# Optimization experiments

Measured on AMD Instinct MI355X. Metric: run time of the kernel, lower is better.

The kernel has to match this reference:

```python
import jax, jax.numpy as jnp
import numpy as np

B, L, A = 16, 32, 2046
M = A + 2  # user col + attributors + item col = 2048 nodes


def _xavier_uniform(key, shape, gain):
    fan_out, fan_in = shape  # torch 2D param: fan_in = shape[1], fan_out = shape[0]
    bound = gain * np.sqrt(6.0 / (fan_in + fan_out))
    return jax.random.uniform(key, shape, jnp.float32, -bound, bound)


def setup_inputs() -> dict:
    key = jax.random.key(0)
    k = jax.random.split(key, 7)
    user = jax.random.normal(k[0], (B, 6 * L, 1), jnp.float32)
    item = jax.random.normal(k[1], (B, 6 * L, 1), jnp.float32)
    attributor = jax.random.normal(k[2], (B, 6 * L, A), jnp.float32)
    adj = (jax.random.uniform(k[3], (M, M)) < 0.5).astype(jnp.float32)
    initial_weight = jax.random.normal(k[4], (M, M), jnp.float32)
    W_1 = _xavier_uniform(k[5], (6 * L, A), gain=np.sqrt(2.0))  # relu gain
    W_2 = _xavier_uniform(k[6], (6 * L, L), gain=1.44)
    return {"user": user, "item": item, "attributor": attributor,
            "adj": adj, "initial_weight": initial_weight,
            "W_1": W_1, "W_2": W_2}


def reference(user, item, attributor, adj, initial_weight, W_1, W_2):
    N = W_2.shape[1]  # = length L
    a = attributor * W_1                                   # (B, 6L, A)
    raw = jnp.concatenate([user, a, item], axis=2)         # (B, 6L, M)
    Q, K, V = jnp.split(raw, 3, axis=1)                    # each (B, 2L, M)
    r = jax.nn.relu
    # (relu(X).T @ W).T  ==  einsum over the 2L dim -> (B, L, M)
    Query = jnp.einsum('bnm,nl->blm', r(Q), W_2[:2 * N])
    Key = jnp.einsum('bnm,nl->blm', r(K), W_2[2 * N:4 * N])
    Value = jnp.einsum('bnm,nl->blm', r(V), W_2[4 * N:])
    # h = Query.mT @ Key * adj * initial_weight  -> (B, M, M)
    h = jnp.einsum('blm,bln->bmn', Query, Key) * adj * initial_weight
    d = h - jnp.swapaxes(h, -1, -2)
    exp_h = jnp.exp(jnp.where(d > 0, 0.0, d))              # exp(min(d, 0))
    causal = exp_h / (exp_h + jnp.swapaxes(exp_h, -1, -2)) * adj  # (B, M, M)
    Ans = Value @ causal                                    # (B, L, M)
    idx = jnp.array([0, Ans.shape[2] - 1])
    return Ans[:, :, idx]                                   # (B, L, 2)
```

## Files before the change

kernel.cpp:

```cpp
#include <hip/hip_runtime.h>
#include <math.h>

#define BB 16
#define LL 32
#define AA 2046
#define MM 2048
#define NROWS 192


__device__ __forceinline__ size_t Pidx(int rc, int j, int b, int n) {
  return ((size_t)(rc * 2 + j) * BB + b) * MM + n;
}

__global__ __launch_bounds__(256) void prep_kernel(
    const float* __restrict__ user, const float* __restrict__ item,
    const float* __restrict__ W2, float* __restrict__ uv,
    float* __restrict__ part) {
  const int b = blockIdx.x, t = threadIdx.x;
  __shared__ float KQ[4][LL];
  __shared__ float uvs[4][64];
  if (t < 128) {
    const int q = t >> 5, l = t & 31;
    const float* __restrict__ src = (q == 0 || q == 2) ? user : item;
    const int rbase = (q < 2) ? 64 : 0;
    float acc = 0.f;
#pragma unroll
    for (int r = 0; r < 64; ++r)
      acc += fmaxf(src[b * NROWS + rbase + r], 0.f) * W2[(rbase + r) * LL + l];
    KQ[q][l] = acc;
  }
  __syncthreads();
  {
    const int which = t >> 6, r = t & 63;
    const int wrow = (which < 2) ? r : 64 + r;
    float acc = 0.f;
#pragma unroll
    for (int l = 0; l < LL; ++l) acc += W2[wrow * LL + l] * KQ[which][l];
    uvs[which][r] = acc;
    uv[which * (BB * 64) + b * 64 + r] = acc;
  }
  __syncthreads();
  if (t < 8) {
    const int nsel = t & 1, j = (t >> 1) & 1, z = t >> 2;
    const float* __restrict__ src = nsel ? item : user;
    float acc = 0.f;
#pragma unroll
    for (int i = 0; i < 64; ++i)
      acc += fmaxf(src[b * NROWS + z * 64 + i], 0.f) * uvs[2 * z + j][i];
    const int n = nsel ? (MM - 1) : 0;
    part[Pidx(2 * z, j, b, n)] = acc;
    part[Pidx(2 * z + 1, j, b, n)] = 0.f;
  }
}

__global__ __launch_bounds__(256) void st_kernel(
    const float* __restrict__ att, const float* __restrict__ W1,
    const float* __restrict__ uv, float* __restrict__ part) {
  const int col = blockIdx.x * 256 + threadIdx.x;
  const int b = blockIdx.y, rc = blockIdx.z;
  if (col >= AA) return;
  const int z = rc >> 1;
  const float* __restrict__ w0 = uv + (2 * z) * (BB * 64) + b * 64;
  const float* __restrict__ w1 = uv + (2 * z + 1) * (BB * 64) + b * 64;
  const int r0 = rc * 32;
  float a0 = 0.f, a1 = 0.f;
#pragma unroll
  for (int i = 0; i < 32; ++i) {
    const int r = r0 + i;
    const float v =
        fmaxf(att[(size_t)(b * NROWS + r) * AA + col] * W1[(size_t)r * AA + col],
              0.f);
    const int wi = r - z * 64;
    a0 += v * w0[wi];
    a1 += v * w1[wi];
  }
  const int n = col + 1;
  part[Pidx(rc, 0, b, n)] = a0;
  part[Pidx(rc, 1, b, n)] = a1;
}

__global__ __launch_bounds__(256) void cweight_kernel(
    const float* __restrict__ adj, const float* __restrict__ iw,
    const float* __restrict__ part, float* __restrict__ c) {
  const int idx = blockIdx.x * 256 + threadIdx.x;
  const int b = idx >> 11, n = idx & (MM - 1);
  const float s0 = part[Pidx(0, 0, b, n)] + part[Pidx(1, 0, b, n)];
  const float s1 = part[Pidx(0, 1, b, n)] + part[Pidx(1, 1, b, n)];
  const float t0 = part[Pidx(2, 0, b, n)] + part[Pidx(3, 0, b, n)];
  const float t1 = part[Pidx(2, 1, b, n)] + part[Pidx(3, 1, b, n)];
  const float an0 = adj[(size_t)n * MM];
  const float an1 = adj[(size_t)n * MM + (MM - 1)];
  const float wn0 = an0 * iw[(size_t)n * MM];
  const float wn1 = an1 * iw[(size_t)n * MM + (MM - 1)];
  const float w0n = adj[n] * iw[n];
  const float w1n =
      adj[(size_t)(MM - 1) * MM + n] * iw[(size_t)(MM - 1) * MM + n];
  const float d0 = s0 * wn0 - t0 * w0n;
  const float d1 = s1 * wn1 - t1 * w1n;
  const float e0 = expf(-fabsf(d0));
  const float e1 = expf(-fabsf(d1));
  const float sig0 = (d0 > 0.f) ? 1.f / (1.f + e0) : e0 / (1.f + e0);
  const float sig1 = (d1 > 0.f) ? 1.f / (1.f + e1) : e1 / (1.f + e1);
  c[b * MM + n] = sig0 * an0;
  c[BB * MM + b * MM + n] = sig1 * an1;
}

__global__ __launch_bounds__(256) void gather_kernel(
    const float* __restrict__ user, const float* __restrict__ item,
    const float* __restrict__ att, const float* __restrict__ W1,
    const float* __restrict__ c, const float* __restrict__ W2,
    float* __restrict__ out) {
  const int rv = blockIdx.x, b = blockIdx.y, tid = threadIdx.x;
  const int r = 128 + rv;
  const int gr = b * NROWS + r;
  const float* __restrict__ c0 = c + b * MM;
  const float* __restrict__ c1 = c + BB * MM + b * MM;
  float g0 = 0.f, g1 = 0.f;
#pragma unroll
  for (int i = 0; i < 8; ++i) {
    const int col = i * 256 + tid;
    if (col < AA) {
      const float v = fmaxf(
          att[(size_t)gr * AA + col] * W1[(size_t)r * AA + col], 0.f);
      g0 += v * c0[col + 1];
      g1 += v * c1[col + 1];
    }
  }
  if (tid == 0) {
    const float uval = fmaxf(user[gr], 0.f);
    const float ival = fmaxf(item[gr], 0.f);
    g0 += uval * c0[0] + ival * c0[MM - 1];
    g1 += uval * c1[0] + ival * c1[MM - 1];
  }
  __shared__ float r0[256], r1[256];
  r0[tid] = g0;
  r1[tid] = g1;
  __syncthreads();
  for (int s = 128; s > 0; s >>= 1) {
    if (tid < s) {
      r0[tid] += r0[tid + s];
      r1[tid] += r1[tid + s];
    }
    __syncthreads();
  }
  if (tid < 64) {
    const int l = tid & 31, j = tid >> 5;
    const float g = j ? r1[0] : r0[0];
    atomicAdd(&out[b * (LL * 2) + l * 2 + j], W2[r * LL + l] * g);
  }
}

extern "C" void kernel_launch(void* const* d_in, const int* in_sizes, int n_in,
                              void* d_out, int out_size, void* d_ws,
                              size_t ws_size, hipStream_t stream) {
  const float* user = (const float*)d_in[0];
  const float* item = (const float*)d_in[1];
  const float* att = (const float*)d_in[2];
  const float* adj = (const float*)d_in[3];
  const float* iw = (const float*)d_in[4];
  const float* W1 = (const float*)d_in[5];
  const float* W2 = (const float*)d_in[6];
  float* out = (float*)d_out;

  float* uv = (float*)d_ws;
  float* part = uv + 4 * BB * 64;
  float* c = part + 8 * BB * MM;

  hipMemsetAsync(d_out, 0, sizeof(float) * (size_t)out_size, stream);

  prep_kernel<<<dim3(BB), 256, 0, stream>>>(user, item, W2, uv, part);
  st_kernel<<<dim3(8, BB, 4), 256, 0, stream>>>(att, W1, uv, part);
  cweight_kernel<<<dim3(BB * MM / 256), 256, 0, stream>>>(adj, iw, part, c);
  gather_kernel<<<dim3(64, BB), 256, 0, stream>>>(user, item, att, W1, c, W2,
                                                  out);
}
```

Measured before the change: 112.7 us.

## Fuse prep, partial-sum and weight kernels via last-block counters

```diff
diff --git a/kernel.cpp b/kernel.cpp
--- a/kernel.cpp
+++ b/kernel.cpp
@@ -8,145 +8,187 @@
 #define NROWS 192
 
 
-__device__ __forceinline__ size_t Pidx(int rc, int j, int b, int n) {
-  return ((size_t)(rc * 2 + j) * BB + b) * MM + n;
-}
-
-__global__ __launch_bounds__(256) void prep_kernel(
+__global__ __launch_bounds__(256) void stc_kernel(
     const float* __restrict__ user, const float* __restrict__ item,
-    const float* __restrict__ W2, float* __restrict__ uv,
-    float* __restrict__ part) {
-  const int b = blockIdx.x, t = threadIdx.x;
-  __shared__ float KQ[4][LL];
-  __shared__ float uvs[4][64];
-  if (t < 128) {
-    const int q = t >> 5, l = t & 31;
-    const float* __restrict__ src = (q == 0 || q == 2) ? user : item;
-    const int rbase = (q < 2) ? 64 : 0;
+    const float* __restrict__ att, const float* __restrict__ W1,
+    const float* __restrict__ W2, const float* __restrict__ adj,
+    const float* __restrict__ iw, int* __restrict__ cnt,
+    float* __restrict__ part, float* __restrict__ bnd, float* __restrict__ c) {
+  const int x = blockIdx.x, b = blockIdx.y, rc = blockIdx.z;
+  const int t = threadIdx.x;
+  const int z = rc >> 1;
+  __shared__ float KQ[2][LL];
+  __shared__ float uvs[2][64];
+  __shared__ int lastflag;
+
+  if (t < 64) {
+    const int j = t >> 5, l = t & 31;
+    const float* __restrict__ src = j ? item : user;
+    const int rbase = (z == 0) ? 64 : 0;
     float acc = 0.f;
 #pragma unroll
     for (int r = 0; r < 64; ++r)
       acc += fmaxf(src[b * NROWS + rbase + r], 0.f) * W2[(rbase + r) * LL + l];
-    KQ[q][l] = acc;
-  }
-  __syncthreads();
-  {
-    const int which = t >> 6, r = t & 63;
-    const int wrow = (which < 2) ? r : 64 + r;
-    float acc = 0.f;
-#pragma unroll
-    for (int l = 0; l < LL; ++l) acc += W2[wrow * LL + l] * KQ[which][l];
-    uvs[which][r] = acc;
-    uv[which * (BB * 64) + b * 64 + r] = acc;
-  }
-  __syncthreads();
-  if (t < 8) {
-    const int nsel = t & 1, j = (t >> 1) & 1, z = t >> 2;
-    const float* __restrict__ src = nsel ? item : user;
-    float acc = 0.f;
-#pragma unroll
-    for (int i = 0; i < 64; ++i)
-      acc += fmaxf(src[b * NROWS + z * 64 + i], 0.f) * uvs[2 * z + j][i];
-    const int n = nsel ? (MM - 1) : 0;
-    part[Pidx(2 * z, j, b, n)] = acc;
-    part[Pidx(2 * z + 1, j, b, n)] = 0.f;
-  }
-}
-
-__global__ __launch_bounds__(256) void st_kernel(
-    const float* __restrict__ att, const float* __restrict__ W1,
-    const float* __restrict__ uv, float* __restrict__ part) {
-  const int col = blockIdx.x * 256 + threadIdx.x;
-  const int b = blockIdx.y, rc = blockIdx.z;
-  if (col >= AA) return;
-  const int z = rc >> 1;
-  const float* __restrict__ w0 = uv + (2 * z) * (BB * 64) + b * 64;
-  const float* __restrict__ w1 = uv + (2 * z + 1) * (BB * 64) + b * 64;
+    KQ[j][l] = acc;
+  }
+  __syncthreads();
+  if (t < 128) {
+    const int j = t >> 6, r = t & 63;
+    const int wrow = (z == 0) ? r : 64 + r;
+    float acc = 0.f;
+#pragma unroll
+    for (int l = 0; l < LL; ++l) acc += W2[wrow * LL + l] * KQ[j][l];
+    uvs[j][r] = acc;
+  }
+  __syncthreads();
+
+  const int col0 = x * 512 + 2 * t;
   const int r0 = rc * 32;
-  float a0 = 0.f, a1 = 0.f;
-#pragma unroll
-  for (int i = 0; i < 32; ++i) {
-    const int r = r0 + i;
-    const float v =
-        fmaxf(att[(size_t)(b * NROWS + r) * AA + col] * W1[(size_t)r * AA + col],
-              0.f);
-    const int wi = r - z * 64;
-    a0 += v * w0[wi];
-    a1 += v * w1[wi];
-  }
-  const int n = col + 1;
-  part[Pidx(rc, 0, b, n)] = a0;
-  part[Pidx(rc, 1, b, n)] = a1;
-}
-
-__global__ __launch_bounds__(256) void cweight_kernel(
-    const float* __restrict__ adj, const float* __restrict__ iw,
-    const float* __restrict__ part, float* __restrict__ c) {
-  const int idx = blockIdx.x * 256 + threadIdx.x;
-  const int b = idx >> 11, n = idx & (MM - 1);
-  const float s0 = part[Pidx(0, 0, b, n)] + part[Pidx(1, 0, b, n)];
-  const float s1 = part[Pidx(0, 1, b, n)] + part[Pidx(1, 1, b, n)];
-  const float t0 = part[Pidx(2, 0, b, n)] + part[Pidx(3, 0, b, n)];
-  const float t1 = part[Pidx(2, 1, b, n)] + part[Pidx(3, 1, b, n)];
-  const float an0 = adj[(size_t)n * MM];
-  const float an1 = adj[(size_t)n * MM + (MM - 1)];
-  const float wn0 = an0 * iw[(size_t)n * MM];
-  const float wn1 = an1 * iw[(size_t)n * MM + (MM - 1)];
-  const float w0n = adj[n] * iw[n];
-  const float w1n =
-      adj[(size_t)(MM - 1) * MM + n] * iw[(size_t)(MM - 1) * MM + n];
-  const float d0 = s0 * wn0 - t0 * w0n;
-  const float d1 = s1 * wn1 - t1 * w1n;
-  const float e0 = expf(-fabsf(d0));
-  const float e1 = expf(-fabsf(d1));
-  const float sig0 = (d0 > 0.f) ? 1.f / (1.f + e0) : e0 / (1.f + e0);
-  const float sig1 = (d1 > 0.f) ? 1.f / (1.f + e1) : e1 / (1.f + e1);
-  c[b * MM + n] = sig0 * an0;
-  c[BB * MM + b * MM + n] = sig1 * an1;
+  const int wibase = r0 - z * 64;
+  if (col0 < AA) {
+    float a00 = 0.f, a01 = 0.f, a10 = 0.f, a11 = 0.f;
+#pragma unroll
+    for (int i = 0; i < 32; ++i) {
+      const int r = r0 + i;
+      const float2 av =
+          ((const float2*)att)[((size_t)(b * NROWS + r) * AA + col0) >> 1];
+      const float2 wv = ((const float2*)W1)[((size_t)r * AA + col0) >> 1];
+      const float v0 = fmaxf(av.x * wv.x, 0.f);
+      const float v1 = fmaxf(av.y * wv.y, 0.f);
+      const float u0 = uvs[0][wibase + i], u1 = uvs[1][wibase + i];
+      a00 += v0 * u0;
+      a01 += v1 * u0;
+      a10 += v0 * u1;
+      a11 += v1 * u1;
+    }
+    float* p0 = part + ((size_t)(rc * 2 + 0) * BB + b) * 2048;
+    float* p1 = part + ((size_t)(rc * 2 + 1) * BB + b) * 2048;
+    ((float2*)p0)[col0 >> 1] = make_float2(a00, a01);
+    ((float2*)p1)[col0 >> 1] = make_float2(a10, a11);
+  }
+
+  if (x == 0 && t >= 128 && t < 132) {
+    const int idx = t - 128, which = idx & 1, j = idx >> 1;
+    const float* __restrict__ src = which ? item : user;
+    float acc = 0.f;
+#pragma unroll
+    for (int i = 0; i < 32; ++i)
+      acc += fmaxf(src[b * NROWS + r0 + i], 0.f) * uvs[j][wibase + i];
+    bnd[((rc * 2 + j) * BB + b) * 2 + which] = acc;
+  }
+
+  __threadfence();
+  __syncthreads();
+  if (t == 0) {
+    const int old = atomicAdd(&cnt[b], 1);
+    lastflag = (old == 16 - 1);
+  }
+  __syncthreads();
+  if (!lastflag) return;
+  __threadfence();
+
+#pragma unroll
+  for (int i = 0; i < 8; ++i) {
+    const int n = i * 256 + t;
+    float s0, s1, t0v, t1v;
+    if (n == 0 || n == MM - 1) {
+      const int which = (n == 0) ? 0 : 1;
+      s0 = bnd[(0 * BB + b) * 2 + which] + bnd[(2 * BB + b) * 2 + which];
+      s1 = bnd[(1 * BB + b) * 2 + which] + bnd[(3 * BB + b) * 2 + which];
+      t0v = bnd[(4 * BB + b) * 2 + which] + bnd[(6 * BB + b) * 2 + which];
+      t1v = bnd[(5 * BB + b) * 2 + which] + bnd[(7 * BB + b) * 2 + which];
+    } else {
+      const int col = n - 1;
+      s0 = part[((size_t)0 * BB + b) * 2048 + col] +
+           part[((size_t)2 * BB + b) * 2048 + col];
+      s1 = part[((size_t)1 * BB + b) * 2048 + col] +
+           part[((size_t)3 * BB + b) * 2048 + col];
+      t0v = part[((size_t)4 * BB + b) * 2048 + col] +
+            part[((size_t)6 * BB + b) * 2048 + col];
+      t1v = part[((size_t)5 * BB + b) * 2048 + col] +
+            part[((size_t)7 * BB + b) * 2048 + col];
+    }
+    const float an0 = adj[(size_t)n * MM];
+    const float an1 = adj[(size_t)n * MM + (MM - 1)];
+    const float wn0 = an0 * iw[(size_t)n * MM];
+    const float wn1 = an1 * iw[(size_t)n * MM + (MM - 1)];
+    const float w0n = adj[n] * iw[n];
+    const float w1n =
+        adj[(size_t)(MM - 1) * MM + n] * iw[(size_t)(MM - 1) * MM + n];
+    const float d0 = s0 * wn0 - t0v * w0n;
+    const float d1 = s1 * wn1 - t1v * w1n;
+    const float e0 = expf(-fabsf(d0));
+    const float e1 = expf(-fabsf(d1));
+    const float sig0 = (d0 > 0.f) ? 1.f / (1.f + e0) : e0 / (1.f + e0);
+    const float sig1 = (d1 > 0.f) ? 1.f / (1.f + e1) : e1 / (1.f + e1);
+    c[b * MM + n] = sig0 * an0;
+    c[BB * MM + b * MM + n] = sig1 * an1;
+  }
 }
 
 __global__ __launch_bounds__(256) void gather_kernel(
     const float* __restrict__ user, const float* __restrict__ item,
     const float* __restrict__ att, const float* __restrict__ W1,
-    const float* __restrict__ c, const float* __restrict__ W2,
-    float* __restrict__ out) {
-  const int rv = blockIdx.x, b = blockIdx.y, tid = threadIdx.x;
+    const float* __restrict__ W2, const float* __restrict__ c,
+    int* __restrict__ cnt, float* __restrict__ gg, float* __restrict__ out) {
+  const int rv = blockIdx.x, b = blockIdx.y, t = threadIdx.x;
   const int r = 128 + rv;
   const int gr = b * NROWS + r;
   const float* __restrict__ c0 = c + b * MM;
   const float* __restrict__ c1 = c + BB * MM + b * MM;
   float g0 = 0.f, g1 = 0.f;
 #pragma unroll
-  for (int i = 0; i < 8; ++i) {
-    const int col = i * 256 + tid;
+  for (int i = 0; i < 4; ++i) {
+    const int col = i * 512 + 2 * t;
     if (col < AA) {
-      const float v = fmaxf(
-          att[(size_t)gr * AA + col] * W1[(size_t)r * AA + col], 0.f);
-      g0 += v * c0[col + 1];
-      g1 += v * c1[col + 1];
+      const float2 av = ((const float2*)att)[((size_t)gr * AA + col) >> 1];
+      const float2 wv = ((const float2*)W1)[((size_t)r * AA + col) >> 1];
+      const float v0 = fmaxf(av.x * wv.x, 0.f);
+      const float v1 = fmaxf(av.y * wv.y, 0.f);
+      g0 += v0 * c0[col + 1] + v1 * c0[col + 2];
+      g1 += v0 * c1[col + 1] + v1 * c1[col + 2];
     }
   }
-  if (tid == 0) {
+  if (t == 0) {
     const float uval = fmaxf(user[gr], 0.f);
     const float ival = fmaxf(item[gr], 0.f);
     g0 += uval * c0[0] + ival * c0[MM - 1];
     g1 += uval * c1[0] + ival * c1[MM - 1];
   }
-  __shared__ float r0[256], r1[256];
-  r0[tid] = g0;
-  r1[tid] = g1;
-  __syncthreads();
-  for (int s = 128; s > 0; s >>= 1) {
-    if (tid < s) {
-      r0[tid] += r0[tid + s];
-      r1[tid] += r1[tid + s];
-    }
-    __syncthreads();
-  }
-  if (tid < 64) {
-    const int l = tid & 31, j = tid >> 5;
-    const float g = j ? r1[0] : r0[0];
-    atomicAdd(&out[b * (LL * 2) + l * 2 + j], W2[r * LL + l] * g);
+#pragma unroll
+  for (int o = 32; o > 0; o >>= 1) {
+    g0 += __shfl_down(g0, o);
+    g1 += __shfl_down(g1, o);
+  }
+  __shared__ float rg[2][4];
+  __shared__ int lastflag;
+  if ((t & 63) == 0) {
+    rg[0][t >> 6] = g0;
+    rg[1][t >> 6] = g1;
+  }
+  __syncthreads();
+  if (t == 0) {
+    const float s0 = rg[0][0] + rg[0][1] + rg[0][2] + rg[0][3];
+    const float s1 = rg[1][0] + rg[1][1] + rg[1][2] + rg[1][3];
+    ((float2*)gg)[b * 64 + rv] = make_float2(s0, s1);
+  }
+  __threadfence();
+  __syncthreads();
+  if (t == 0) {
+    const int old = atomicAdd(&cnt[16 + b], 1);
+    lastflag = (old == 64 - 1);
+  }
+  __syncthreads();
+  if (!lastflag) return;
+  __threadfence();
+
+  if (t < 64) {
+    const int l = t & 31, j = t >> 5;
+    float acc = 0.f;
+#pragma unroll
+    for (int i = 0; i < 64; ++i)
+      acc += W2[(128 + i) * LL + l] * gg[(b * 64 + i) * 2 + j];
+    out[b * 64 + l * 2 + j] = acc;
   }
 }
 
@@ -162,15 +204,16 @@
   const float* W2 = (const float*)d_in[6];
   float* out = (float*)d_out;
 
-  float* uv = (float*)d_ws;
-  float* part = uv + 4 * BB * 64;
-  float* c = part + 8 * BB * MM;
-
-  hipMemsetAsync(d_out, 0, sizeof(float) * (size_t)out_size, stream);
-
-  prep_kernel<<<dim3(BB), 256, 0, stream>>>(user, item, W2, uv, part);
-  st_kernel<<<dim3(8, BB, 4), 256, 0, stream>>>(att, W1, uv, part);
-  cweight_kernel<<<dim3(BB * MM / 256), 256, 0, stream>>>(adj, iw, part, c);
-  gather_kernel<<<dim3(64, BB), 256, 0, stream>>>(user, item, att, W1, c, W2,
-                                                  out);
+  int* cnt = (int*)d_ws;
+  float* part = (float*)d_ws + 32;
+  float* bnd = part + 262144;
+  float* c = bnd + 256;
+  float* gg = c + 65536;
+
+  hipMemsetAsync(cnt, 0, 32 * sizeof(int), stream);
+
+  stc_kernel<<<dim3(4, BB, 4), 256, 0, stream>>>(user, item, att, W1, W2, adj,
+                                                 iw, cnt, part, bnd, c);
+  gather_kernel<<<dim3(64, BB), 256, 0, stream>>>(user, item, att, W1, W2, c,
+                                                  cnt, gg, out);
 }
```

Result: slower. 212.7 us (+88.7%).
